# Kernel optimization log

Hardware: AMD Instinct MI355X
Metric: run time of the kernel (lower is better)

Reference implementation:

```python
import jax, jax.numpy as jnp
import numpy as np

B, S, D, H = 2, 2048, 1024, 16
EPS = 1e-7  # keras backend epsilon

def setup_inputs() -> dict:
    key = jax.random.key(0)
    ks = jax.random.split(key, 5)
    x = jax.random.normal(ks[0], (B, S, D), dtype=jnp.float32)
    # mem_mask convention: attend where mem_mask == 0 (causal here)
    i = jnp.arange(S)
    causal = (i[None, :] > i[:, None]).astype(jnp.float32)  # 1 = masked
    mem_mask = jnp.broadcast_to(causal[None, None], (B, 1, S, S))
    Wqkv = jax.random.normal(ks[1], (D, 3 * D), dtype=jnp.float32) * (D ** -0.5)
    W_out = jax.random.normal(ks[2], (D, D), dtype=jnp.float32) * (D ** -0.5)
    b_out = jnp.zeros((D,), dtype=jnp.float32)
    scale = jnp.ones((D,), dtype=jnp.float32)
    gate = jax.random.normal(ks[3], (D,), dtype=jnp.float32) * 0.02
    return {"x": x, "mem_mask": mem_mask, "Wqkv": Wqkv, "W_out": W_out,
            "b_out": b_out, "scale": scale, "gate": gate}

def reference(x, mem_mask, Wqkv, W_out, b_out, scale, gate):
    b, s, d = x.shape
    dh = d // H
    h = jnp.einsum('bsd,de->bse', x, Wqkv)
    q, k, v = jnp.split(h, 3, axis=-1)
    def split_heads(t):
        return t.reshape(b, s, H, dh).transpose(0, 2, 1, 3)  # [B,H,S,dh]
    q, k, v = split_heads(q), split_heads(k), split_heads(v)
    q = q * (dh ** -0.5)
    logits = jnp.einsum('bhqd,bhkd->bhqk', q, k)
    logits = logits * (mem_mask == 0.0).astype(logits.dtype)
    weights = jax.nn.relu(logits)
    o = jnp.einsum('bhqk,bhkd->bhqd', weights, v)
    o = o.transpose(0, 2, 1, 3).reshape(b, s, d)  # combine heads
    # Gated RMSNorm
    ms = jnp.mean(o * o, axis=-1, keepdims=True)
    o = scale * o * jax.lax.rsqrt(ms + EPS) * jax.nn.sigmoid(gate * o)
    return jnp.einsum('bsd,de->bse', o, W_out) + b_out
```

## Files before the change

### kernel.cpp

```cpp
#include <hip/hip_runtime.h>
#include <hip/hip_bf16.h>

typedef unsigned short u16;
typedef __attribute__((ext_vector_type(8))) short bf16x8;
typedef __attribute__((ext_vector_type(4))) short short4v;
typedef __attribute__((ext_vector_type(4))) float floatx4;
typedef __attribute__((ext_vector_type(2))) unsigned uint2v;
typedef __attribute__((ext_vector_type(4))) unsigned uint4v;

__device__ __forceinline__ float bf2f(u16 u) {
    unsigned v = ((unsigned)u) << 16;
    return __builtin_bit_cast(float, v);
}
__device__ __forceinline__ u16 f2bf(float f) {
    unsigned u = __builtin_bit_cast(unsigned, f);
    u += 0x7fffu + ((u >> 16) & 1u);
    return (u16)(u >> 16);
}

#define GLDS16(g, l)                                                             \
    __builtin_amdgcn_global_load_lds(                                            \
        (const __attribute__((address_space(1))) void*)(g),                      \
        (__attribute__((address_space(3))) void*)(l), 16, 0, 0)

__device__ __forceinline__ uint2v pl32(unsigned a, unsigned b) {
#if __has_builtin(__builtin_amdgcn_permlane32_swap)
    auto r = __builtin_amdgcn_permlane32_swap(a, b, false, false);
    uint2v o; o.x = (unsigned)r[0]; o.y = (unsigned)r[1]; return o;
#else
    unsigned as = (unsigned)__shfl_xor((int)a, 32, 64);
    unsigned bs = (unsigned)__shfl_xor((int)b, 32, 64);
    const bool hi = (threadIdx.x & 32) != 0;
    uint2v o; o.x = hi ? bs : a; o.y = hi ? b : as; return o;
#endif
}
__device__ __forceinline__ uint2v pl16(unsigned a, unsigned b) {
#if __has_builtin(__builtin_amdgcn_permlane16_swap)
    auto r = __builtin_amdgcn_permlane16_swap(a, b, false, false);
    uint2v o; o.x = (unsigned)r[0]; o.y = (unsigned)r[1]; return o;
#else
    unsigned as = (unsigned)__shfl_xor((int)a, 16, 64);
    unsigned bs = (unsigned)__shfl_xor((int)b, 16, 64);
    const bool odd = (threadIdx.x & 16) != 0;
    uint2v o; o.x = odd ? bs : a; o.y = odd ? b : as; return o;
#endif
}

__global__ __launch_bounds__(256) void prep(const float* __restrict__ x, u16* __restrict__ xb,
                                            const float* __restrict__ Wqkv, u16* __restrict__ WqkvT,
                                            const float* __restrict__ Wout, u16* __restrict__ WoutT) {
    __shared__ u16 t[32][33];
    int blk = blockIdx.x;
    if (blk < 4096) {
        const int i = blk * 256 + threadIdx.x;
        const floatx4 v = ((const floatx4*)x)[i];
        short4v o;
#pragma unroll
        for (int j = 0; j < 4; ++j) o[j] = (short)f2bf(v[j]);
        ((short4v*)xb)[i] = o;
        return;
    }
    const float* in; u16* out; int R, C, bx, by;
    if (blk < 4096 + 3072) { blk -= 4096; in = Wqkv; out = WqkvT; R = 1024; C = 3072; bx = blk % 96; by = blk / 96; }
    else                   { blk -= 7168; in = Wout; out = WoutT; R = 1024; C = 1024; bx = blk & 31; by = blk >> 5; }
    const int c0 = bx * 32, r0 = by * 32;
    const int xx = threadIdx.x & 31, yy = threadIdx.x >> 5;
#pragma unroll
    for (int i = 0; i < 32; i += 8) t[yy + i][xx] = f2bf(in[(size_t)(r0 + yy + i) * C + c0 + xx]);
    __syncthreads();
#pragma unroll
    for (int i = 0; i < 32; i += 8) out[(size_t)(c0 + yy + i) * R + r0 + xx] = t[xx][yy + i];
}

__global__ __launch_bounds__(256, 3) void gemm_qkv(const u16* __restrict__ A, const u16* __restrict__ Bt,
                                                   u16* __restrict__ C, u16* __restrict__ vtp) {
    constexpr int K = 1024, N = 3072;
    __shared__ u16 sA[3][128 * 32];
    __shared__ u16 sB[3][128 * 32];
    const int tid = threadIdx.x;
    const int lane = tid & 63, wave = tid >> 6;
    const int l15 = lane & 15, quad = lane >> 4;
    const int row0 = blockIdx.y * 128, col0 = blockIdx.x * 128;
    const int wm = (wave & 1) * 64, wn = (wave >> 1) * 64;

    const u16* aq[2]; const u16* bq[2]; int lo[2];
#pragma unroll
    for (int it = 0; it < 2; ++it) {
        const int idx = it * 256 + tid;
        const int r = idx >> 2, bb = idx & 3;
        const int c = bb ^ ((r >> 1) & 3);
        aq[it] = A + (size_t)(row0 + r) * K + c * 8;
        bq[it] = Bt + (size_t)(col0 + r) * K + c * 8;
        lo[it] = idx * 8;
    }
    auto stage = [&](int bufi) {
#pragma unroll
        for (int it = 0; it < 2; ++it) {
            GLDS16(aq[it], &sA[bufi][lo[it]]);
            GLDS16(bq[it], &sB[bufi][lo[it]]);
            aq[it] += 32; bq[it] += 32;
        }
    };

    floatx4 acc[4][4] = {};
    stage(0); stage(1);
    int bc = 0, bn = 1, bs = 2;
    for (int kc = 0; kc < 32; ++kc) {
        if (kc < 31) asm volatile("s_waitcnt vmcnt(4)" ::: "memory");
        else         asm volatile("s_waitcnt vmcnt(0)" ::: "memory");
        __builtin_amdgcn_s_barrier();
        asm volatile("" ::: "memory");
        __builtin_amdgcn_sched_barrier(0);
        if (kc + 2 < 32) stage(bs);

        const u16* sa = sA[bc];
        const u16* sb = sB[bc];
        __builtin_amdgcn_s_setprio(1);
        bf16x8 af[4], bfr[4];
#pragma unroll
        for (int j = 0; j < 4; ++j) {
            const int r = wn + j * 16 + l15;
            const int s = r * 4 + (quad ^ ((r >> 1) & 3));
            bfr[j] = *(const bf16x8*)(sb + s * 8);
        }
#pragma unroll
        for (int i = 0; i < 4; ++i) {
            const int r = wm + i * 16 + l15;
            const int s = r * 4 + (quad ^ ((r >> 1) & 3));
            af[i] = *(const bf16x8*)(sa + s * 8);
        }
#pragma unroll
        for (int i = 0; i < 4; ++i)
#pragma unroll
            for (int j = 0; j < 4; ++j)
                acc[i][j] = __builtin_amdgcn_mfma_f32_16x16x32_bf16(af[i], bfr[j], acc[i][j], 0, 0, 0);
        __builtin_amdgcn_s_setprio(0);
        int t_ = bc; bc = bn; bn = bs; bs = t_;
    }
#pragma unroll
    for (int i = 0; i < 4; ++i) {
#pragma unroll
        for (int j = 0; j < 4; ++j) {
            const int col = col0 + wn + j * 16 + l15;
            const int row = row0 + wm + i * 16 + quad * 4;
#pragma unroll
            for (int r = 0; r < 4; ++r)
                C[(size_t)(row + r) * N + col] = f2bf(acc[i][j][r]);
            if (col0 >= 2048) {
                short4v pk;
#pragma unroll
                for (int r = 0; r < 4; ++r) pk[r] = (short)f2bf(acc[i][j][r] * 0.125f);
                const int bb2 = row >> 11, s = row & 2047;
                const int hd = (col - 2048) >> 6, dh = col & 63;
                *(short4v*)(vtp + ((size_t)(bb2 * 16 + hd) * 64 + dh) * 2048 + s) = pk;
            }
        }
    }
}

template <int TM, int BN, bool BIAS, typename OUT>
__global__ __launch_bounds__(256) void gemm_bt(const u16* __restrict__ A, const u16* __restrict__ Bt,
                                               OUT* __restrict__ C, const float* __restrict__ bias,
                                               int M, int N, int K) {
    constexpr int MI = TM / 32;
    constexpr int NJ = BN / 32;
    __shared__ u16 sA[TM * 32];
    __shared__ u16 sB[BN * 32];
    const int tid = threadIdx.x;
    const int lane = tid & 63, wave = tid >> 6;
    const int l15 = lane & 15, quad = lane >> 4;
    const int row0 = blockIdx.y * TM, col0 = blockIdx.x * BN;
    const int wm = (wave & 1) * (TM / 2), wn = (wave >> 1) * (BN / 2);
    const int c_ = (tid & 3) << 3;
    floatx4 acc[MI][NJ] = {};
    for (int k0 = 0; k0 < K; k0 += 32) {
#pragma unroll
        for (int it = 0; it < BN / 64; ++it) {
            const int idx = it * 256 + tid;
            const int r = idx >> 2;
            GLDS16(Bt + (size_t)(col0 + r) * K + k0 + c_, sB + idx * 8);
        }
#pragma unroll
        for (int it = 0; it < TM / 64; ++it) {
            const int idx = it * 256 + tid;
            const int r = idx >> 2;
            GLDS16(A + (size_t)(row0 + r) * K + k0 + c_, sA + idx * 8);
        }
        __syncthreads();
        bf16x8 af[MI], bfr[NJ];
#pragma unroll
        for (int i = 0; i < MI; ++i) af[i] = *(const bf16x8*)(sA + (wm + i * 16 + l15) * 32 + quad * 8);
#pragma unroll
        for (int j = 0; j < NJ; ++j) bfr[j] = *(const bf16x8*)(sB + (wn + j * 16 + l15) * 32 + quad * 8);
#pragma unroll
        for (int i = 0; i < MI; ++i)
#pragma unroll
            for (int j = 0; j < NJ; ++j)
                acc[i][j] = __builtin_amdgcn_mfma_f32_16x16x32_bf16(af[i], bfr[j], acc[i][j], 0, 0, 0);
        __syncthreads();
    }
#pragma unroll
    for (int i = 0; i < MI; ++i) {
#pragma unroll
        for (int j = 0; j < NJ; ++j) {
            const int col = col0 + wn + j * 16 + l15;
            const int row = row0 + wm + i * 16 + quad * 4;
            const float b = BIAS ? bias[col] : 0.f;
#pragma unroll
            for (int r = 0; r < 4; ++r) {
                const float v = acc[i][j][r] + b;
                if constexpr (sizeof(OUT) == 2)
                    C[(size_t)(row + r) * N + col] = (OUT)f2bf(v);
                else
                    C[(size_t)(row + r) * N + col] = (OUT)v;
            }
        }
    }
}

__device__ __forceinline__ uint2v pack_relu(floatx4 s, bool diag, int kgb, int qg) {
    float v0 = fmaxf(s[0], 0.f), v1 = fmaxf(s[1], 0.f);
    float v2 = fmaxf(s[2], 0.f), v3 = fmaxf(s[3], 0.f);
    if (diag) {
        if (kgb + 0 > qg) v0 = 0.f;
        if (kgb + 1 > qg) v1 = 0.f;
        if (kgb + 2 > qg) v2 = 0.f;
        if (kgb + 3 > qg) v3 = 0.f;
    }
    uint2v p;
    p.x = ((__builtin_bit_cast(unsigned, v0) + 0x8000u) >> 16) |
          ((__builtin_bit_cast(unsigned, v1) + 0x8000u) & 0xffff0000u);
    p.y = ((__builtin_bit_cast(unsigned, v2) + 0x8000u) >> 16) |
          ((__builtin_bit_cast(unsigned, v3) + 0x8000u) & 0xffff0000u);
    return p;
}

__device__ __forceinline__ bf16x8 pfrag(uint2v A, uint2v B) {
    uint2v gx = pl32(A.x, B.x);
    uint2v dx = pl16(gx.x, gx.y);
    uint2v gy = pl32(A.y, B.y);
    uint2v dy = pl16(gy.x, gy.y);
    uint4v w; w.x = dx.x; w.y = dy.x; w.z = dx.y; w.w = dy.y;
    return __builtin_bit_cast(bf16x8, w);
}

__global__ __launch_bounds__(256, 2) void relu_attn(const u16* __restrict__ h, const u16* __restrict__ vt,
                                                    float* __restrict__ o) {
    union SM {
        struct { u16 K[2][128 * 64]; u16 V[2][64 * 128]; } kv;
        float red[4][64 * 68];
    };
    __shared__ SM sm;
    const int bid = blockIdx.x;
    const int pr = bid >> 5;
    const int bh = bid & 31;
    const int qt64 = 31 - pr;
    const int b = bh >> 4, hd = bh & 15;
    const int tid = threadIdx.x, lane = tid & 63, wave = tid >> 6;
    const int l15 = lane & 15, quad = lane >> 4;
    const int nc = (qt64 >> 1) + 1;

    const int qrow0 = b * 2048 + qt64 * 64;
    bf16x8 qf[4][2];
#pragma unroll
    for (int qt = 0; qt < 4; ++qt)
#pragma unroll
        for (int ks = 0; ks < 2; ++ks)
            qf[qt][ks] = *(const bf16x8*)(h + (size_t)(qrow0 + qt * 16 + l15) * 3072 + hd * 64 + ks * 32 + quad * 8);

    floatx4 acc[4][4] = {};

    const u16* kbase = h + (size_t)(b * 2048) * 3072 + 1024 + hd * 64;
    const u16* vbase = vt + (size_t)bh * 64 * 2048;

    const u16* kq[4]; const u16* vq[4]; int klo[4], vlo[4];
#pragma unroll
    for (int it = 0; it < 4; ++it) {
        const int idx = it * 256 + tid;
        { const int r = idx >> 3, c = idx & 7, cg = c ^ (r & 7);
          kq[it] = kbase + (size_t)r * 3072 + cg * 8; klo[it] = idx * 8; }
        { const int r = idx >> 4, c = idx & 15, cg = c ^ (r & 15);
          vq[it] = vbase + (size_t)r * 2048 + cg * 8; vlo[it] = idx * 8; }
    }
    auto stage = [&](int bufi) {
#pragma unroll
        for (int it = 0; it < 4; ++it) { GLDS16(kq[it], &sm.kv.K[bufi][klo[it]]); kq[it] += 128 * 3072; }
#pragma unroll
        for (int it = 0; it < 4; ++it) { GLDS16(vq[it], &sm.kv.V[bufi][vlo[it]]); vq[it] += 128; }
    };

    stage(0);
    int buf = 0;
    for (int kc = 0; kc < nc; ++kc) {
        asm volatile("s_waitcnt vmcnt(0)" ::: "memory");
        __builtin_amdgcn_s_barrier();
        asm volatile("" ::: "memory");
        __builtin_amdgcn_sched_barrier(0);
        if (kc + 1 < nc) stage(buf ^ 1);

        const u16* sK = sm.kv.K[buf];
        const u16* sV = sm.kv.V[buf];
        __builtin_amdgcn_s_setprio(1);
        bf16x8 kf[2][2];
#pragma unroll
        for (int kt = 0; kt < 2; ++kt)
#pragma unroll
            for (int ks = 0; ks < 2; ++ks) {
                const int row = wave * 32 + kt * 16 + l15;
                const int blk = (quad + ks * 4) ^ (row & 7);
                kf[kt][ks] = *(const bf16x8*)(sK + row * 64 + blk * 8);
            }
        const floatx4 z = {0.f, 0.f, 0.f, 0.f};
        floatx4 s[2][4];
#pragma unroll
        for (int kt = 0; kt < 2; ++kt)
#pragma unroll
            for (int qt = 0; qt < 4; ++qt) {
                floatx4 t = __builtin_amdgcn_mfma_f32_16x16x32_bf16(kf[kt][0], qf[qt][0], z, 0, 0, 0);
                s[kt][qt] = __builtin_amdgcn_mfma_f32_16x16x32_bf16(kf[kt][1], qf[qt][1], t, 0, 0, 0);
            }
        const bool last = (kc == nc - 1);
        uint2v p[2][4];
#pragma unroll
        for (int kt = 0; kt < 2; ++kt)
#pragma unroll
            for (int qt = 0; qt < 4; ++qt)
                p[kt][qt] = pack_relu(s[kt][qt], last,
                                      kc * 128 + wave * 32 + kt * 16 + quad * 4,
                                      qt64 * 64 + qt * 16 + l15);
        bf16x8 vf[4];
#pragma unroll
        for (int nt = 0; nt < 4; ++nt) {
            const int row = nt * 16 + l15;
            const int blk = (wave * 4 + quad) ^ (row & 15);
            vf[nt] = *(const bf16x8*)(sV + row * 128 + blk * 8);
        }
#pragma unroll
        for (int qt = 0; qt < 4; ++qt) {
            const bf16x8 pa = pfrag(p[0][qt], p[1][qt]);
#pragma unroll
            for (int nt = 0; nt < 4; ++nt)
                acc[qt][nt] = __builtin_amdgcn_mfma_f32_16x16x32_bf16(pa, vf[nt], acc[qt][nt], 0, 0, 0);
        }
        __builtin_amdgcn_s_setprio(0);
        buf ^= 1;
    }

    __syncthreads();
    float* rw = sm.red[wave];
#pragma unroll
    for (int qt = 0; qt < 4; ++qt)
#pragma unroll
        for (int nt = 0; nt < 4; ++nt) {
            const int d = nt * 16 + l15, q = qt * 16 + quad * 4;
            *(floatx4*)(rw + d * 68 + q) = acc[qt][nt];
        }
    __syncthreads();
    {
        const int d = lane;
#pragma unroll
        for (int j = 0; j < 4; ++j) {
            const int q = wave * 16 + j * 4;
            floatx4 a = *(const floatx4*)(sm.red[0] + d * 68 + q);
            a += *(const floatx4*)(sm.red[1] + d * 68 + q);
            a += *(const floatx4*)(sm.red[2] + d * 68 + q);
            a += *(const floatx4*)(sm.red[3] + d * 68 + q);
#pragma unroll
            for (int jj = 0; jj < 4; ++jj)
                o[(size_t)(qrow0 + q + jj) * 1024 + hd * 64 + d] = a[jj];
        }
    }
}

__global__ __launch_bounds__(256) void rms_gate(const float* __restrict__ o, const float* __restrict__ scale,
                                                const float* __restrict__ gate, u16* __restrict__ out) {
    const int row = blockIdx.x;
    const int tid = threadIdx.x;
    const floatx4* op = (const floatx4*)(o + (size_t)row * 1024);
    floatx4 v = op[tid];
    float ss = v[0] * v[0] + v[1] * v[1] + v[2] * v[2] + v[3] * v[3];
#pragma unroll
    for (int m = 32; m >= 1; m >>= 1) ss += __shfl_xor(ss, m, 64);
    __shared__ float red[4];
    if ((tid & 63) == 0) red[tid >> 6] = ss;
    __syncthreads();
    const float ms = (red[0] + red[1] + red[2] + red[3]) * (1.0f / 1024.0f);
    const float inv = rsqrtf(ms + 1e-7f);
    const int c = tid * 4;
#pragma unroll
    for (int j = 0; j < 4; ++j) {
        const float s = scale[c + j];
        const float g = gate[c + j];
        const float x = v[j];
        const float sig = 1.0f / (1.0f + __expf(-g * x));
        out[(size_t)row * 1024 + c + j] = f2bf(s * x * inv * sig);
    }
}

extern "C" void kernel_launch(void* const* d_in, const int* in_sizes, int n_in,
                              void* d_out, int out_size, void* d_ws, size_t ws_size,
                              hipStream_t stream) {
    const float* x     = (const float*)d_in[0];
    const float* Wqkv  = (const float*)d_in[2];
    const float* Wout  = (const float*)d_in[3];
    const float* bout  = (const float*)d_in[4];
    const float* scale = (const float*)d_in[5];
    const float* gate  = (const float*)d_in[6];
    float* out = (float*)d_out;

    char* p = (char*)d_ws;
    u16* xb    = (u16*)p; p += (size_t)4096 * 1024 * 2;
    u16* h     = (u16*)p; p += (size_t)4096 * 3072 * 2;
    u16* vt    = (u16*)p; p += (size_t)32 * 64 * 2048 * 2;
    u16* WqkvT = (u16*)p; p += (size_t)3072 * 1024 * 2;
    u16* WoutT = (u16*)p; p += (size_t)1024 * 1024 * 2;
    float* oat = (float*)p; p += (size_t)4096 * 1024 * 4;
    u16* onorm = (u16*)p; p += (size_t)4096 * 1024 * 2;

    prep<<<8192, 256, 0, stream>>>(x, xb, Wqkv, WqkvT, Wout, WoutT);
    gemm_qkv<<<dim3(24, 32), 256, 0, stream>>>(xb, WqkvT, h, vt);
    relu_attn<<<1024, 256, 0, stream>>>(h, vt, oat);
    rms_gate<<<4096, 256, 0, stream>>>(oat, scale, gate, onorm);
    gemm_bt<128, 64, true, float><<<dim3(16, 32), 256, 0, stream>>>(onorm, WoutT, out, bout, 4096, 1024, 1024);
}
```

Baseline: 200.8 us.

## Pipeline output GEMM with triple-buffered swizzled LDS and remap GEMM block order

Replaces the generic single-buffered output projection GEMM with a specialized kernel that uses three LDS buffers, async global-to-LDS loads overlapped with MFMA, an XOR swizzle to avoid bank conflicts, and raised wave priority. It also remaps block indices for both the QKV and output GEMMs to a 1D grid with an 8-way interleave, so that blocks spread across XCDs share operand tiles in cache. The aim is to hide load latency and improve L2 reuse. The cost is more LDS per block, which may lower occupancy.

```diff
diff --git a/kernel.cpp b/kernel.cpp
--- a/kernel.cpp
+++ b/kernel.cpp
@@ -80,7 +80,10 @@
     const int tid = threadIdx.x;
     const int lane = tid & 63, wave = tid >> 6;
     const int l15 = lane & 15, quad = lane >> 4;
-    const int row0 = blockIdx.y * 128, col0 = blockIdx.x * 128;
+    const int bid = blockIdx.x;
+    const int sw = (bid & 7) * 96 + (bid >> 3);
+    const int bx = sw % 24, by = sw / 24;
+    const int row0 = by * 128, col0 = bx * 128;
     const int wm = (wave & 1) * 64, wn = (wave >> 1) * 64;
 
     const u16* aq[2]; const u16* bq[2]; int lo[2];
@@ -158,62 +161,86 @@
     }
 }
 
-template <int TM, int BN, bool BIAS, typename OUT>
-__global__ __launch_bounds__(256) void gemm_bt(const u16* __restrict__ A, const u16* __restrict__ Bt,
-                                               OUT* __restrict__ C, const float* __restrict__ bias,
-                                               int M, int N, int K) {
-    constexpr int MI = TM / 32;
-    constexpr int NJ = BN / 32;
-    __shared__ u16 sA[TM * 32];
-    __shared__ u16 sB[BN * 32];
+__global__ __launch_bounds__(256, 2) void gemm_out(const u16* __restrict__ A, const u16* __restrict__ Bt,
+                                                   float* __restrict__ C, const float* __restrict__ bias) {
+    constexpr int K = 1024, N = 1024;
+    __shared__ u16 sA[3][128 * 32];
+    __shared__ u16 sB[3][64 * 32];
     const int tid = threadIdx.x;
     const int lane = tid & 63, wave = tid >> 6;
     const int l15 = lane & 15, quad = lane >> 4;
-    const int row0 = blockIdx.y * TM, col0 = blockIdx.x * BN;
-    const int wm = (wave & 1) * (TM / 2), wn = (wave >> 1) * (BN / 2);
-    const int c_ = (tid & 3) << 3;
-    floatx4 acc[MI][NJ] = {};
-    for (int k0 = 0; k0 < K; k0 += 32) {
-#pragma unroll
-        for (int it = 0; it < BN / 64; ++it) {
-            const int idx = it * 256 + tid;
-            const int r = idx >> 2;
-            GLDS16(Bt + (size_t)(col0 + r) * K + k0 + c_, sB + idx * 8);
-        }
-#pragma unroll
-        for (int it = 0; it < TM / 64; ++it) {
-            const int idx = it * 256 + tid;
-            const int r = idx >> 2;
-            GLDS16(A + (size_t)(row0 + r) * K + k0 + c_, sA + idx * 8);
-        }
-        __syncthreads();
-        bf16x8 af[MI], bfr[NJ];
-#pragma unroll
-        for (int i = 0; i < MI; ++i) af[i] = *(const bf16x8*)(sA + (wm + i * 16 + l15) * 32 + quad * 8);
-#pragma unroll
-        for (int j = 0; j < NJ; ++j) bfr[j] = *(const bf16x8*)(sB + (wn + j * 16 + l15) * 32 + quad * 8);
-#pragma unroll
-        for (int i = 0; i < MI; ++i)
-#pragma unroll
-            for (int j = 0; j < NJ; ++j)
+    const int bid = blockIdx.x;
+    const int sw = (bid & 7) * 64 + (bid >> 3);
+    const int bx = sw & 15, by = sw >> 4;
+    const int row0 = by * 128, col0 = bx * 64;
+    const int wm = (wave & 1) * 64, wn = (wave >> 1) * 32;
+
+    const u16* aq[2]; const u16* bq; int lo[2], lob;
+#pragma unroll
+    for (int it = 0; it < 2; ++it) {
+        const int idx = it * 256 + tid;
+        const int r = idx >> 2, bb = idx & 3;
+        const int c = bb ^ ((r >> 1) & 3);
+        aq[it] = A + (size_t)(row0 + r) * K + c * 8;
+        lo[it] = idx * 8;
+    }
+    {
+        const int r = tid >> 2, bb = tid & 3;
+        const int c = bb ^ ((r >> 1) & 3);
+        bq = Bt + (size_t)(col0 + r) * K + c * 8;
+        lob = tid * 8;
+    }
+    auto stage = [&](int bufi) {
+        GLDS16(aq[0], &sA[bufi][lo[0]]); aq[0] += 32;
+        GLDS16(aq[1], &sA[bufi][lo[1]]); aq[1] += 32;
+        GLDS16(bq, &sB[bufi][lob]); bq += 32;
+    };
+
+    floatx4 acc[4][2] = {};
+    stage(0); stage(1);
+    int bc = 0, bn = 1, bs = 2;
+    for (int kc = 0; kc < 32; ++kc) {
+        if (kc < 31) asm volatile("s_waitcnt vmcnt(3)" ::: "memory");
+        else         asm volatile("s_waitcnt vmcnt(0)" ::: "memory");
+        __builtin_amdgcn_s_barrier();
+        asm volatile("" ::: "memory");
+        __builtin_amdgcn_sched_barrier(0);
+        if (kc + 2 < 32) stage(bs);
+
+        const u16* sa = sA[bc];
+        const u16* sb = sB[bc];
+        __builtin_amdgcn_s_setprio(1);
+        bf16x8 af[4], bfr[2];
+#pragma unroll
+        for (int j = 0; j < 2; ++j) {
+            const int r = wn + j * 16 + l15;
+            const int s = r * 4 + (quad ^ ((r >> 1) & 3));
+            bfr[j] = *(const bf16x8*)(sb + s * 8);
+        }
+#pragma unroll
+        for (int i = 0; i < 4; ++i) {
+            const int r = wm + i * 16 + l15;
+            const int s = r * 4 + (quad ^ ((r >> 1) & 3));
+            af[i] = *(const bf16x8*)(sa + s * 8);
+        }
+#pragma unroll
+        for (int i = 0; i < 4; ++i)
+#pragma unroll
+            for (int j = 0; j < 2; ++j)
                 acc[i][j] = __builtin_amdgcn_mfma_f32_16x16x32_bf16(af[i], bfr[j], acc[i][j], 0, 0, 0);
-        __syncthreads();
-    }
-#pragma unroll
-    for (int i = 0; i < MI; ++i) {
-#pragma unroll
-        for (int j = 0; j < NJ; ++j) {
+        __builtin_amdgcn_s_setprio(0);
+        int t_ = bc; bc = bn; bn = bs; bs = t_;
+    }
+#pragma unroll
+    for (int i = 0; i < 4; ++i) {
+#pragma unroll
+        for (int j = 0; j < 2; ++j) {
             const int col = col0 + wn + j * 16 + l15;
             const int row = row0 + wm + i * 16 + quad * 4;
-            const float b = BIAS ? bias[col] : 0.f;
-#pragma unroll
-            for (int r = 0; r < 4; ++r) {
-                const float v = acc[i][j][r] + b;
-                if constexpr (sizeof(OUT) == 2)
-                    C[(size_t)(row + r) * N + col] = (OUT)f2bf(v);
-                else
-                    C[(size_t)(row + r) * N + col] = (OUT)v;
-            }
+            const float b = bias[col];
+#pragma unroll
+            for (int r = 0; r < 4; ++r)
+                C[(size_t)(row + r) * N + col] = acc[i][j][r] + b;
         }
     }
 }
@@ -418,8 +445,8 @@
     u16* onorm = (u16*)p; p += (size_t)4096 * 1024 * 2;
 
     prep<<<8192, 256, 0, stream>>>(x, xb, Wqkv, WqkvT, Wout, WoutT);
-    gemm_qkv<<<dim3(24, 32), 256, 0, stream>>>(xb, WqkvT, h, vt);
+    gemm_qkv<<<768, 256, 0, stream>>>(xb, WqkvT, h, vt);
     relu_attn<<<1024, 256, 0, stream>>>(h, vt, oat);
     rms_gate<<<4096, 256, 0, stream>>>(oat, scale, gate, onorm);
-    gemm_bt<128, 64, true, float><<<dim3(16, 32), 256, 0, stream>>>(onorm, WoutT, out, bout, 4096, 1024, 1024);
-}
+    gemm_out<<<512, 256, 0, stream>>>(onorm, WoutT, out, bout);
+}
```

After: 197.0 us (median of 2 runs). Within noise of the previous version (-1.9%).
